# Optimization experiments

Measured on AMD Instinct MI355X. Metric: run time of the kernel, lower is better.

Reference implementation:

```python
import jax, jax.numpy as jnp
import numpy as np

N = 50000      # nodes
E = 500000     # edges
IN = 128       # input feature dim
HID = 64       # hidden per-head dim
CLS = 64       # num classes
SLOPE = 0.2    # leaky_relu negative slope


def _gat_layer(x, W, al, ar, src, dst):
    """One GATConv: project, per-edge score, edge-softmax over dst, weighted aggregate.
    x: [N, Din], W: [Din, H*F], al/ar: [H, F]. Returns [N, H, F]."""
    H, F = al.shape
    n = x.shape[0]
    feat = (x @ W).reshape(n, H, F)                      # [N,H,F]
    el = jnp.einsum('nhf,hf->nh', feat, al)              # [N,H]
    er = jnp.einsum('nhf,hf->nh', feat, ar)              # [N,H]
    e = el[src] + er[dst]                                # u_add_v -> [E,H]
    e = jnp.where(e >= 0, e, SLOPE * e)                  # leaky_relu
    # edge_softmax over destination nodes (numerically stable)
    m = jax.lax.stop_gradient(jax.ops.segment_max(e, dst, num_segments=n))
    ex = jnp.exp(e - m[dst])
    denom = jax.ops.segment_sum(ex, dst, num_segments=n)
    a = ex / denom[dst]                                  # [E,H]
    # u_mul_e + sum aggregation
    out = jax.ops.segment_sum(feat[src] * a[:, :, None], dst, num_segments=n)
    return out                                           # [N,H,F]


def setup_inputs() -> dict:
    key = jax.random.key(0)
    ks = jax.random.split(key, 12)
    s = 0.05  # xavier-ish scale
    x = jax.random.normal(ks[0], (N, IN), jnp.float32)
    src = jax.random.randint(ks[1], (E,), 0, N)
    dst = jax.random.randint(ks[2], (E,), 0, N)
    W1 = jax.random.normal(ks[3], (IN, 4 * HID), jnp.float32) * s
    al1 = jax.random.normal(ks[4], (4, HID), jnp.float32) * s
    ar1 = jax.random.normal(ks[5], (4, HID), jnp.float32) * s
    W2 = jax.random.normal(ks[6], (4 * HID, 4 * HID), jnp.float32) * s
    al2 = jax.random.normal(ks[7], (4, HID), jnp.float32) * s
    ar2 = jax.random.normal(ks[8], (4, HID), jnp.float32) * s
    W3 = jax.random.normal(ks[9], (4 * HID, CLS), jnp.float32) * s
    al3 = jax.random.normal(ks[10], (1, CLS), jnp.float32) * s
    ar3 = jax.random.normal(ks[11], (1, CLS), jnp.float32) * s
    res_W3 = jax.random.normal(jax.random.fold_in(key, 99), (4 * HID, CLS), jnp.float32) * s
    return {"x": x, "W1": W1, "al1": al1, "ar1": ar1, "W2": W2, "al2": al2,
            "ar2": ar2, "W3": W3, "al3": al3, "ar3": ar3, "res_W3": res_W3,
            "src": src, "dst": dst}


def reference(x, W1, al1, ar1, W2, al2, ar2, W3, al3, ar3, res_W3, src, dst):
    # layer 0: no residual, elu activation, flatten heads
    h = _gat_layer(x, W1, al1, ar1, src, dst)            # [N,4,64]
    h = jax.nn.elu(h).reshape(N, -1)                     # [N,256]
    # layer 1: residual is Identity (in_dst 256 == 4*64), elu, flatten
    h1 = _gat_layer(h, W2, al2, ar2, src, dst)           # [N,4,64]
    h1 = h1 + h.reshape(N, 4, HID)                       # residual (Identity)
    h = jax.nn.elu(h1).reshape(N, -1)                    # [N,256]
    # layer 2: residual Linear 256->64, no activation, mean over heads
    h2 = _gat_layer(h, W3, al3, ar3, src, dst)           # [N,1,64]
    h2 = h2 + (h @ res_W3).reshape(N, 1, CLS)            # residual fc
    logits = h2.mean(axis=1)                             # [N,64]
    return logits
```

## Files before the change

kernel.cpp:

```cpp
#include <hip/hip_runtime.h>
#include <hip/hip_bf16.h>
#include <math.h>

#define SLOPE 0.2f

typedef __attribute__((ext_vector_type(8))) short short8;
typedef __attribute__((ext_vector_type(4))) float f32x4;

static __device__ __forceinline__ float leakyf(float x) { return x >= 0.f ? x : SLOPE * x; }
static __device__ __forceinline__ float bflo(unsigned u) { return __builtin_bit_cast(float, u << 16); }
static __device__ __forceinline__ float bfhi(unsigned u) { return __builtin_bit_cast(float, u & 0xffff0000u); }
static __device__ __forceinline__ unsigned short f2bf(float f) {
    unsigned u = __builtin_bit_cast(unsigned, f);
    return (unsigned short)((u + 0x7fff + ((u >> 16) & 1)) >> 16);
}

struct __align__(8) us4 { unsigned short a, b, c, d; };

__global__ __launch_bounds__(256) void tconv_all(const float* __restrict__ W1,
                                                 const float* __restrict__ W2,
                                                 const float* __restrict__ W3,
                                                 const float* __restrict__ rW3,
                                                 unsigned short* __restrict__ W1t,
                                                 unsigned short* __restrict__ W2t,
                                                 unsigned short* __restrict__ W3c) {
    int i = blockIdx.x * 256 + threadIdx.x;
    const float* W; unsigned short* Wt; int K, lNc, idx;
    if (i < 32768)       { W = W1;  Wt = W1t;            K = 128; lNc = 8; idx = i; }
    else if (i < 98304)  { W = W2;  Wt = W2t;            K = 256; lNc = 8; idx = i - 32768; }
    else if (i < 114688) { W = W3;  Wt = W3c;            K = 256; lNc = 6; idx = i - 98304; }
    else                 { W = rW3; Wt = W3c + 64 * 256; K = 256; lNc = 6; idx = i - 114688; }
    int k = idx >> lNc, n = idx & ((1 << lNc) - 1);
    Wt[n * K + k] = f2bf(W[idx]);
}

template<bool A_F32>
__global__ __launch_bounds__(256) void gemm_l12(const void* __restrict__ Av,
                                                const unsigned short* __restrict__ Wt,
                                                unsigned short* __restrict__ outb,
                                                const float* __restrict__ al,
                                                const float* __restrict__ ar,
                                                float* __restrict__ el,
                                                float* __restrict__ er,
                                                int M, int K) {
    const int lane = threadIdx.x & 63;
    const int wid = threadIdx.x >> 6;
    const int rlo = lane & 15;
    const int q = lane >> 4;
    const int kg = q * 8;
    const int m0 = blockIdx.x * 64;
    const int cbase = wid * 64;

    f32x4 acc[4][4];
#pragma unroll
    for (int mf = 0; mf < 4; ++mf)
#pragma unroll
        for (int nf = 0; nf < 4; ++nf) acc[mf][nf] = (f32x4){0.f, 0.f, 0.f, 0.f};

    for (int k0 = 0; k0 < K; k0 += 32) {
        short8 a[4];
#pragma unroll
        for (int mf = 0; mf < 4; ++mf) {
            int r = m0 + mf * 16 + rlo;
            if (r >= M) r = M - 1;
            if (A_F32) {
                const float* ap = (const float*)Av + (size_t)r * K + k0 + kg;
                float4 f0 = *(const float4*)ap;
                float4 f1 = *(const float4*)(ap + 4);
                short8 t;
                t[0] = f2bf(f0.x); t[1] = f2bf(f0.y); t[2] = f2bf(f0.z); t[3] = f2bf(f0.w);
                t[4] = f2bf(f1.x); t[5] = f2bf(f1.y); t[6] = f2bf(f1.z); t[7] = f2bf(f1.w);
                a[mf] = t;
            } else {
                a[mf] = *(const short8*)((const unsigned short*)Av + (size_t)r * K + k0 + kg);
            }
        }
#pragma unroll
        for (int nf = 0; nf < 4; ++nf) {
            short8 b = *(const short8*)(Wt + (size_t)(cbase + nf * 16 + rlo) * K + k0 + kg);
#pragma unroll
            for (int mf = 0; mf < 4; ++mf)
                acc[mf][nf] = __builtin_amdgcn_mfma_f32_16x16x32_bf16(a[mf], b, acc[mf][nf], 0, 0, 0);
        }
    }

    float alv[4], arv[4];
#pragma unroll
    for (int nf = 0; nf < 4; ++nf) {
        alv[nf] = al[cbase + nf * 16 + rlo];
        arv[nf] = ar[cbase + nf * 16 + rlo];
    }

#pragma unroll
    for (int mf = 0; mf < 4; ++mf) {
#pragma unroll
        for (int reg = 0; reg < 4; ++reg) {
            int r = m0 + mf * 16 + q * 4 + reg;
            float pl = 0.f, pr = 0.f;
#pragma unroll
            for (int nf = 0; nf < 4; ++nf) {
                pl += acc[mf][nf][reg] * alv[nf];
                pr += acc[mf][nf][reg] * arv[nf];
            }
#pragma unroll
            for (int off = 1; off < 16; off <<= 1) {
                pl += __shfl_xor(pl, off);
                pr += __shfl_xor(pr, off);
            }
            if (rlo == 0 && r < M) {
                el[(size_t)r * 4 + wid] = pl;
                er[(size_t)r * 4 + wid] = pr;
            }
            if (r < M) {
#pragma unroll
                for (int nf = 0; nf < 4; ++nf)
                    outb[(size_t)r * 256 + cbase + nf * 16 + rlo] = f2bf(acc[mf][nf][reg]);
            }
        }
    }
}

__global__ __launch_bounds__(256) void gemm_l3(const unsigned short* __restrict__ A,
                                               const unsigned short* __restrict__ Wt,
                                               unsigned short* __restrict__ featb,
                                               float* __restrict__ resf,
                                               const float* __restrict__ al,
                                               const float* __restrict__ ar,
                                               float* __restrict__ el,
                                               float* __restrict__ er, int M) {
    const int K = 256;
    const int lane = threadIdx.x & 63;
    const int wid = threadIdx.x >> 6;
    const int rlo = lane & 15;
    const int q = lane >> 4;
    const int kg = q * 8;
    const int m0 = blockIdx.x * 128 + (wid >> 1) * 64;
    const int ch = wid & 1;
    const int cbase = ch * 64;

    f32x4 acc[4][4];
#pragma unroll
    for (int mf = 0; mf < 4; ++mf)
#pragma unroll
        for (int nf = 0; nf < 4; ++nf) acc[mf][nf] = (f32x4){0.f, 0.f, 0.f, 0.f};

    for (int k0 = 0; k0 < K; k0 += 32) {
        short8 a[4];
#pragma unroll
        for (int mf = 0; mf < 4; ++mf) {
            int r = m0 + mf * 16 + rlo;
            if (r >= M) r = M - 1;
            a[mf] = *(const short8*)(A + (size_t)r * K + k0 + kg);
        }
#pragma unroll
        for (int nf = 0; nf < 4; ++nf) {
            short8 b = *(const short8*)(Wt + (size_t)(cbase + nf * 16 + rlo) * K + k0 + kg);
#pragma unroll
            for (int mf = 0; mf < 4; ++mf)
                acc[mf][nf] = __builtin_amdgcn_mfma_f32_16x16x32_bf16(a[mf], b, acc[mf][nf], 0, 0, 0);
        }
    }

    float alv[4], arv[4];
    if (ch == 0) {
#pragma unroll
        for (int nf = 0; nf < 4; ++nf) {
            alv[nf] = al[nf * 16 + rlo];
            arv[nf] = ar[nf * 16 + rlo];
        }
    }

#pragma unroll
    for (int mf = 0; mf < 4; ++mf) {
#pragma unroll
        for (int reg = 0; reg < 4; ++reg) {
            int r = m0 + mf * 16 + q * 4 + reg;
            if (ch == 0) {
                float pl = 0.f, pr = 0.f;
#pragma unroll
                for (int nf = 0; nf < 4; ++nf) {
                    pl += acc[mf][nf][reg] * alv[nf];
                    pr += acc[mf][nf][reg] * arv[nf];
                }
#pragma unroll
                for (int off = 1; off < 16; off <<= 1) {
                    pl += __shfl_xor(pl, off);
                    pr += __shfl_xor(pr, off);
                }
                if (rlo == 0 && r < M) { el[r] = pl; er[r] = pr; }
                if (r < M) {
#pragma unroll
                    for (int nf = 0; nf < 4; ++nf)
                        featb[(size_t)r * 64 + nf * 16 + rlo] = f2bf(acc[mf][nf][reg]);
                }
            } else if (r < M) {
#pragma unroll
                for (int nf = 0; nf < 4; ++nf)
                    resf[(size_t)r * 64 + nf * 16 + rlo] = acc[mf][nf][reg];
            }
        }
    }
}

__global__ void hist_kernel(const int* __restrict__ dst, int* __restrict__ counts, int e) {
    int i = blockIdx.x * blockDim.x + threadIdx.x;
    if (i < e) atomicAdd(&counts[dst[i]], 1);
}

__global__ __launch_bounds__(1024) void scan_block(const int* __restrict__ counts,
                                                   int* __restrict__ offsets,
                                                   int* __restrict__ bsums, int n) {
    __shared__ int ws[16];
    int tid = threadIdx.x, lane = tid & 63, wid = tid >> 6;
    int idx = blockIdx.x * 1024 + tid;
    int v = (idx < n) ? counts[idx] : 0;
    int s = v;
#pragma unroll
    for (int off = 1; off < 64; off <<= 1) {
        int t = __shfl_up(s, off);
        if (lane >= off) s += t;
    }
    if (lane == 63) ws[wid] = s;
    __syncthreads();
    if (tid < 16) {
        int w2 = ws[tid];
#pragma unroll
        for (int off = 1; off < 16; off <<= 1) {
            int t = __shfl_up(w2, off);
            if (tid >= off) w2 += t;
        }
        ws[tid] = w2;
    }
    __syncthreads();
    int wpre = wid ? ws[wid - 1] : 0;
    if (idx < n) offsets[idx] = wpre + s - v;
    if (tid == 0) bsums[blockIdx.x] = ws[15];
}

__global__ __launch_bounds__(1024) void add_off(const int* __restrict__ bsums,
                                                int* __restrict__ offsets,
                                                int* __restrict__ cursor, int n, int e, int nb) {
    __shared__ int base_s;
    int tid = threadIdx.x;
    if (tid < 64) {
        int v = (tid < blockIdx.x && tid < nb) ? bsums[tid] : 0;
#pragma unroll
        for (int off = 32; off > 0; off >>= 1) v += __shfl_xor(v, off);
        if (tid == 0) base_s = v;
    }
    __syncthreads();
    int idx = blockIdx.x * 1024 + tid;
    if (idx < n) {
        int v = offsets[idx] + base_s;
        offsets[idx] = v;
        cursor[idx] = v;
    }
    if (idx == 0) offsets[n] = e;
}

__global__ void scatter_kernel(const int* __restrict__ src, const int* __restrict__ dst,
                               int* __restrict__ cursor, int* __restrict__ csr_src, int e) {
    int i = blockIdx.x * blockDim.x + threadIdx.x;
    if (i < e) {
        int pos = atomicAdd(&cursor[dst[i]], 1);
        csr_src[pos] = src[i];
    }
}

template<int H, int RES, int ACT, bool OUT_BF16>
__global__ __launch_bounds__(256) void gat_agg(const unsigned short* __restrict__ fp,
                                               const float* __restrict__ el,
                                               const float* __restrict__ er,
                                               const int* __restrict__ offsets,
                                               const int* __restrict__ csr_src,
                                               const void* __restrict__ resid,
                                               void* __restrict__ outv, int n) {
    const int D = H * 64;
    const int CH = (H == 4) ? 16 : 64;
    __shared__ float lw[4][64];
    __shared__ int ls[4][64];
    int node = blockIdx.x * 4 + (threadIdx.x >> 6);
    int lane = threadIdx.x & 63;
    int wv = threadIdx.x >> 6;
    if (node >= n) return;
    int e0 = offsets[node], e1 = offsets[node + 1];
    const int hs = (H == 4) ? (lane & 3) : 0;
    const int hf = (H == 4) ? (lane >> 4) : 0;
    const int js = (H == 4) ? (lane >> 2) : lane;
    float er_s = er[(size_t)node * H + hs];

    float den = 0.f;
    float acc[4] = {0.f, 0.f, 0.f, 0.f};

    int e = e0;
    while (e < e1) {
        int cnt = e1 - e;
        if (cnt > CH) cnt = CH;
        float w = 0.f;
        int s = 0;
        if (js < cnt) {
            s = csr_src[e + js];
            float xx = fminf(leakyf(el[(size_t)s * H + hs] + er_s), 80.f);
            w = __expf(xx);
        }
        lw[wv][lane] = w;
        if (H == 4) { if (hs == 0) ls[wv][js] = s; }
        else ls[wv][lane] = s;
        asm volatile("s_waitcnt lgkmcnt(0)" ::: "memory");

        int j = 0;
        for (; j + 2 <= cnt; j += 2) {
            float w0 = lw[wv][(H == 4) ? (j * 4 + hf) : j];
            float w1 = lw[wv][(H == 4) ? ((j + 1) * 4 + hf) : (j + 1)];
            int s0 = ls[wv][j], s1 = ls[wv][j + 1];
            den += w0 + w1;
            if (H == 4) {
                uint2 u0 = *(const uint2*)(fp + (size_t)s0 * D + lane * 4);
                uint2 u1 = *(const uint2*)(fp + (size_t)s1 * D + lane * 4);
                acc[0] += w0 * bflo(u0.x) + w1 * bflo(u1.x);
                acc[1] += w0 * bfhi(u0.x) + w1 * bfhi(u1.x);
                acc[2] += w0 * bflo(u0.y) + w1 * bflo(u1.y);
                acc[3] += w0 * bfhi(u0.y) + w1 * bfhi(u1.y);
            } else {
                acc[0] += w0 * bflo((unsigned)fp[(size_t)s0 * D + lane])
                        + w1 * bflo((unsigned)fp[(size_t)s1 * D + lane]);
            }
        }
        if (j < cnt) {
            float w0 = lw[wv][(H == 4) ? (j * 4 + hf) : j];
            int s0 = ls[wv][j];
            den += w0;
            if (H == 4) {
                uint2 u0 = *(const uint2*)(fp + (size_t)s0 * D + lane * 4);
                acc[0] += w0 * bflo(u0.x);
                acc[1] += w0 * bfhi(u0.x);
                acc[2] += w0 * bflo(u0.y);
                acc[3] += w0 * bfhi(u0.y);
            } else {
                acc[0] += w0 * bflo((unsigned)fp[(size_t)s0 * D + lane]);
            }
        }
        e += cnt;
    }

    float inv = den > 0.f ? 1.f / den : 0.f;
    float v[4];
#pragma unroll
    for (int i = 0; i < 4; ++i) v[i] = acc[i] * inv;

    if (RES == 1) {
        uint2 ru = *(const uint2*)((const unsigned short*)resid + (size_t)node * D + lane * 4);
        v[0] += bflo(ru.x); v[1] += bfhi(ru.x); v[2] += bflo(ru.y); v[3] += bfhi(ru.y);
    } else if (RES == 2) {
        v[0] += ((const float*)resid)[(size_t)node * D + lane];
    }
    if (ACT == 1) {
#pragma unroll
        for (int i = 0; i < 4; ++i) v[i] = v[i] > 0.f ? v[i] : __expf(v[i]) - 1.f;
    }
    if (OUT_BF16) {
        if (H == 4) {
            us4 o = {f2bf(v[0]), f2bf(v[1]), f2bf(v[2]), f2bf(v[3])};
            *(us4*)((unsigned short*)outv + (size_t)node * D + lane * 4) = o;
        } else {
            ((unsigned short*)outv)[(size_t)node * D + lane] = f2bf(v[0]);
        }
    } else {
        if (H == 4) {
            float4 o = {v[0], v[1], v[2], v[3]};
            *(float4*)((float*)outv + (size_t)node * D + lane * 4) = o;
        } else {
            ((float*)outv)[(size_t)node * D + lane] = v[0];
        }
    }
}

extern "C" void kernel_launch(void* const* d_in, const int* in_sizes, int n_in,
                              void* d_out, int out_size, void* d_ws, size_t ws_size,
                              hipStream_t stream) {
    const float* x      = (const float*)d_in[0];
    const float* W1     = (const float*)d_in[1];
    const float* al1    = (const float*)d_in[2];
    const float* ar1    = (const float*)d_in[3];
    const float* W2     = (const float*)d_in[4];
    const float* al2    = (const float*)d_in[5];
    const float* ar2    = (const float*)d_in[6];
    const float* W3     = (const float*)d_in[7];
    const float* al3    = (const float*)d_in[8];
    const float* ar3    = (const float*)d_in[9];
    const float* res_W3 = (const float*)d_in[10];
    const int*   src    = (const int*)d_in[11];
    const int*   dst    = (const int*)d_in[12];

    const int N = in_sizes[0] / 128;
    const int E = in_sizes[11];

    float* out = (float*)d_out;

    unsigned short* featb = (unsigned short*)d_ws;
    unsigned short* h1    = featb + (size_t)N * 256;
    unsigned short* h2    = h1 + (size_t)N * 256;
    unsigned short* W1t   = h2 + (size_t)N * 256;
    unsigned short* W2t   = W1t + 256 * 128;
    unsigned short* W3c   = W2t + 256 * 256;
    float* resf = (float*)(W3c + 128 * 256);
    float* el   = resf + (size_t)N * 64;
    float* er   = el + (size_t)N * 4;
    int* offsets = (int*)(er + (size_t)N * 4);
    int* cursor  = offsets + (N + 1);
    int* csr_src = cursor + N;
    int* bsums   = csr_src + E;

    const int T = 256;
    const int scan_blocks = (N + 1023) / 1024;

    tconv_all<<<512, T, 0, stream>>>(W1, W2, W3, res_W3, W1t, W2t, W3c);

    hipMemsetAsync(cursor, 0, (size_t)N * sizeof(int), stream);
    hist_kernel<<<(E + T - 1) / T, T, 0, stream>>>(dst, cursor, E);
    scan_block<<<scan_blocks, 1024, 0, stream>>>(cursor, offsets, bsums, N);
    add_off<<<scan_blocks, 1024, 0, stream>>>(bsums, offsets, cursor, N, E, scan_blocks);
    scatter_kernel<<<(E + T - 1) / T, T, 0, stream>>>(src, dst, cursor, csr_src, E);

    int gemm12_blocks = (N + 63) / 64;
    int gemm3_blocks = (N + 127) / 128;
    int node_blocks = (N + 3) / 4;

    gemm_l12<true><<<gemm12_blocks, T, 0, stream>>>(x, W1t, featb, al1, ar1, el, er, N, 128);
    gat_agg<4, 0, 1, true><<<node_blocks, T, 0, stream>>>(featb, el, er, offsets, csr_src, nullptr, h1, N);

    gemm_l12<false><<<gemm12_blocks, T, 0, stream>>>(h1, W2t, featb, al2, ar2, el, er, N, 256);
    gat_agg<4, 1, 1, true><<<node_blocks, T, 0, stream>>>(featb, el, er, offsets, csr_src, h1, h2, N);

    gemm_l3<<<gemm3_blocks, T, 0, stream>>>(h2, W3c, featb, resf, al3, ar3, el, er, N);
    gat_agg<1, 2, 0, false><<<node_blocks, T, 0, stream>>>(featb, el, er, offsets, csr_src, resf, out, N);
}
```

Before: 284.9 us.

## Precompute edge attention weights in separate kernel and unroll gather by eight

Moves the per-edge leaky-relu and exp score computation out of the aggregation kernel into a new edge-parallel kernel that writes weights in CSR order, using a new csr_dst array filled during scatter. The aggregation loop drops its LDS staging and barrier and instead issues eight independent row gathers per iteration for more memory-level parallelism. This adds three extra launches and an extra E×4 float write and read per layer, and redundant clamped loads on tail iterations.

Measured after the change: 297.6 us. +4.5%, slower.

```diff
diff --git a/kernel.cpp b/kernel.cpp
--- a/kernel.cpp
+++ b/kernel.cpp
@@ -259,88 +259,93 @@
 }
 
 __global__ void scatter_kernel(const int* __restrict__ src, const int* __restrict__ dst,
-                               int* __restrict__ cursor, int* __restrict__ csr_src, int e) {
+                               int* __restrict__ cursor, int* __restrict__ csr_src,
+                               int* __restrict__ csr_dst, int e) {
     int i = blockIdx.x * blockDim.x + threadIdx.x;
     if (i < e) {
-        int pos = atomicAdd(&cursor[dst[i]], 1);
+        int d = dst[i];
+        int pos = atomicAdd(&cursor[d], 1);
         csr_src[pos] = src[i];
+        csr_dst[pos] = d;
+    }
+}
+
+template<int H>
+__global__ __launch_bounds__(256) void edge_scores(const int* __restrict__ csr_src,
+                                                   const int* __restrict__ csr_dst,
+                                                   const float* __restrict__ el,
+                                                   const float* __restrict__ er,
+                                                   float* __restrict__ w, int E) {
+    int e = blockIdx.x * 256 + threadIdx.x;
+    if (e >= E) return;
+    int s = csr_src[e], d = csr_dst[e];
+    if (H == 4) {
+        float4 l = *(const float4*)(el + (size_t)s * 4);
+        float4 r = *(const float4*)(er + (size_t)d * 4);
+        float4 o;
+        o.x = __expf(fminf(leakyf(l.x + r.x), 80.f));
+        o.y = __expf(fminf(leakyf(l.y + r.y), 80.f));
+        o.z = __expf(fminf(leakyf(l.z + r.z), 80.f));
+        o.w = __expf(fminf(leakyf(l.w + r.w), 80.f));
+        *(float4*)(w + (size_t)e * 4) = o;
+    } else {
+        w[e] = __expf(fminf(leakyf(el[s] + er[d]), 80.f));
     }
 }
 
 template<int H, int RES, int ACT, bool OUT_BF16>
 __global__ __launch_bounds__(256) void gat_agg(const unsigned short* __restrict__ fp,
-                                               const float* __restrict__ el,
-                                               const float* __restrict__ er,
+                                               const float* __restrict__ wbuf,
                                                const int* __restrict__ offsets,
                                                const int* __restrict__ csr_src,
                                                const void* __restrict__ resid,
                                                void* __restrict__ outv, int n) {
     const int D = H * 64;
-    const int CH = (H == 4) ? 16 : 64;
-    __shared__ float lw[4][64];
-    __shared__ int ls[4][64];
     int node = blockIdx.x * 4 + (threadIdx.x >> 6);
     int lane = threadIdx.x & 63;
-    int wv = threadIdx.x >> 6;
     if (node >= n) return;
     int e0 = offsets[node], e1 = offsets[node + 1];
-    const int hs = (H == 4) ? (lane & 3) : 0;
     const int hf = (H == 4) ? (lane >> 4) : 0;
-    const int js = (H == 4) ? (lane >> 2) : lane;
-    float er_s = er[(size_t)node * H + hs];
 
     float den = 0.f;
     float acc[4] = {0.f, 0.f, 0.f, 0.f};
 
-    int e = e0;
-    while (e < e1) {
-        int cnt = e1 - e;
-        if (cnt > CH) cnt = CH;
-        float w = 0.f;
-        int s = 0;
-        if (js < cnt) {
-            s = csr_src[e + js];
-            float xx = fminf(leakyf(el[(size_t)s * H + hs] + er_s), 80.f);
-            w = __expf(xx);
-        }
-        lw[wv][lane] = w;
-        if (H == 4) { if (hs == 0) ls[wv][js] = s; }
-        else ls[wv][lane] = s;
-        asm volatile("s_waitcnt lgkmcnt(0)" ::: "memory");
-
-        int j = 0;
-        for (; j + 2 <= cnt; j += 2) {
-            float w0 = lw[wv][(H == 4) ? (j * 4 + hf) : j];
-            float w1 = lw[wv][(H == 4) ? ((j + 1) * 4 + hf) : (j + 1)];
-            int s0 = ls[wv][j], s1 = ls[wv][j + 1];
-            den += w0 + w1;
-            if (H == 4) {
-                uint2 u0 = *(const uint2*)(fp + (size_t)s0 * D + lane * 4);
-                uint2 u1 = *(const uint2*)(fp + (size_t)s1 * D + lane * 4);
-                acc[0] += w0 * bflo(u0.x) + w1 * bflo(u1.x);
-                acc[1] += w0 * bfhi(u0.x) + w1 * bfhi(u1.x);
-                acc[2] += w0 * bflo(u0.y) + w1 * bflo(u1.y);
-                acc[3] += w0 * bfhi(u0.y) + w1 * bfhi(u1.y);
-            } else {
-                acc[0] += w0 * bflo((unsigned)fp[(size_t)s0 * D + lane])
-                        + w1 * bflo((unsigned)fp[(size_t)s1 * D + lane]);
-            }
-        }
-        if (j < cnt) {
-            float w0 = lw[wv][(H == 4) ? (j * 4 + hf) : j];
-            int s0 = ls[wv][j];
-            den += w0;
-            if (H == 4) {
-                uint2 u0 = *(const uint2*)(fp + (size_t)s0 * D + lane * 4);
-                acc[0] += w0 * bflo(u0.x);
-                acc[1] += w0 * bfhi(u0.x);
-                acc[2] += w0 * bflo(u0.y);
-                acc[3] += w0 * bfhi(u0.y);
-            } else {
-                acc[0] += w0 * bflo((unsigned)fp[(size_t)s0 * D + lane]);
-            }
-        }
-        e += cnt;
+    for (int e = e0; e < e1; e += 8) {
+        int s[8];
+        float w[8];
+#pragma unroll
+        for (int j = 0; j < 8; ++j) {
+            int idx = e + j;
+            bool ok = idx < e1;
+            int ii = ok ? idx : (e1 - 1);
+            s[j] = csr_src[ii];
+            float wv = (H == 4) ? wbuf[(size_t)ii * 4 + hf] : wbuf[ii];
+            w[j] = ok ? wv : 0.f;
+        }
+        if (H == 4) {
+            uint2 u[8];
+#pragma unroll
+            for (int j = 0; j < 8; ++j)
+                u[j] = *(const uint2*)(fp + (size_t)s[j] * 256 + lane * 4);
+#pragma unroll
+            for (int j = 0; j < 8; ++j) {
+                den += w[j];
+                acc[0] += w[j] * bflo(u[j].x);
+                acc[1] += w[j] * bfhi(u[j].x);
+                acc[2] += w[j] * bflo(u[j].y);
+                acc[3] += w[j] * bfhi(u[j].y);
+            }
+        } else {
+            unsigned u[8];
+#pragma unroll
+            for (int j = 0; j < 8; ++j)
+                u[j] = ((const unsigned short*)fp)[(size_t)s[j] * 64 + lane];
+#pragma unroll
+            for (int j = 0; j < 8; ++j) {
+                den += w[j];
+                acc[0] += w[j] * bflo(u[j]);
+            }
+        }
     }
 
     float inv = den > 0.f ? 1.f / den : 0.f;
@@ -406,32 +411,38 @@
     float* resf = (float*)(W3c + 128 * 256);
     float* el   = resf + (size_t)N * 64;
     float* er   = el + (size_t)N * 4;
-    int* offsets = (int*)(er + (size_t)N * 4);
+    float* wbuf = er + (size_t)N * 4;
+    int* offsets = (int*)(wbuf + (size_t)E * 4);
     int* cursor  = offsets + (N + 1);
     int* csr_src = cursor + N;
-    int* bsums   = csr_src + E;
+    int* csr_dst = csr_src + E;
+    int* bsums   = csr_dst + E;
 
     const int T = 256;
     const int scan_blocks = (N + 1023) / 1024;
+    const int edge_blocks = (E + T - 1) / T;
 
     tconv_all<<<512, T, 0, stream>>>(W1, W2, W3, res_W3, W1t, W2t, W3c);
 
     hipMemsetAsync(cursor, 0, (size_t)N * sizeof(int), stream);
-    hist_kernel<<<(E + T - 1) / T, T, 0, stream>>>(dst, cursor, E);
+    hist_kernel<<<edge_blocks, T, 0, stream>>>(dst, cursor, E);
     scan_block<<<scan_blocks, 1024, 0, stream>>>(cursor, offsets, bsums, N);
     add_off<<<scan_blocks, 1024, 0, stream>>>(bsums, offsets, cursor, N, E, scan_blocks);
-    scatter_kernel<<<(E + T - 1) / T, T, 0, stream>>>(src, dst, cursor, csr_src, E);
+    scatter_kernel<<<edge_blocks, T, 0, stream>>>(src, dst, cursor, csr_src, csr_dst, E);
 
     int gemm12_blocks = (N + 63) / 64;
     int gemm3_blocks = (N + 127) / 128;
     int node_blocks = (N + 3) / 4;
 
     gemm_l12<true><<<gemm12_blocks, T, 0, stream>>>(x, W1t, featb, al1, ar1, el, er, N, 128);
-    gat_agg<4, 0, 1, true><<<node_blocks, T, 0, stream>>>(featb, el, er, offsets, csr_src, nullptr, h1, N);
+    edge_scores<4><<<edge_blocks, T, 0, stream>>>(csr_src, csr_dst, el, er, wbuf, E);
+    gat_agg<4, 0, 1, true><<<node_blocks, T, 0, stream>>>(featb, wbuf, offsets, csr_src, nullptr, h1, N);
 
     gemm_l12<false><<<gemm12_blocks, T, 0, stream>>>(h1, W2t, featb, al2, ar2, el, er, N, 256);
-    gat_agg<4, 1, 1, true><<<node_blocks, T, 0, stream>>>(featb, el, er, offsets, csr_src, h1, h2, N);
+    edge_scores<4><<<edge_blocks, T, 0, stream>>>(csr_src, csr_dst, el, er, wbuf, E);
+    gat_agg<4, 1, 1, true><<<node_blocks, T, 0, stream>>>(featb, wbuf, offsets, csr_src, h1, h2, N);
 
     gemm_l3<<<gemm3_blocks, T, 0, stream>>>(h2, W3c, featb, resf, al3, ar3, el, er, N);
-    gat_agg<1, 2, 0, false><<<node_blocks, T, 0, stream>>>(featb, el, er, offsets, csr_src, resf, out, N);
-}
+    edge_scores<1><<<edge_blocks, T, 0, stream>>>(csr_src, csr_dst, el, er, wbuf, E);
+    gat_agg<1, 2, 0, false><<<node_blocks, T, 0, stream>>>(featb, wbuf, offsets, csr_src, resf, out, N);
+}
```
